# Performance work log

Measured on AMD Instinct MI355X. Metric: run time of the kernel, lower is better.

Reference implementation:

```python
import jax, jax.numpy as jnp
import numpy as np

B, N, M, P, LQK, LV, DQK, DV = 2, 512, 50, 2, 9, 9, 32, 32
K = DQK // 2  # theta frequencies; repeat_interleave(theta,2) must match last dim of q/k


def setup_inputs() -> dict:
    key = jax.random.key(0)
    ks = jax.random.split(key, 7)
    q = jax.random.normal(ks[0], (B, N, P, LQK, DQK), dtype=jnp.float32)
    k = jax.random.normal(ks[1], (B, N, P, LQK, DQK), dtype=jnp.float32)
    v = jax.random.normal(ks[2], (B, N, P, LV, DV), dtype=jnp.float32)
    pos = jax.random.normal(ks[3], (B, N, 3), dtype=jnp.float32) * 3.0  # atom coords
    u = jax.random.normal(ks[4], (B, M, 3), dtype=jnp.float32)
    grid_u = u / jnp.linalg.norm(u, axis=-1, keepdims=True)  # unit-sphere Lebedev points
    grid_w = jax.random.uniform(ks[5], (B, M), dtype=jnp.float32) / M  # quadrature weights
    theta = jax.random.uniform(ks[6], (K,), dtype=jnp.float32)
    return {"q": q, "k": k, "v": v, "pos": pos, "grid_u": grid_u, "grid_w": grid_w, "theta": theta}


def apply_erope(x, pos, grid_u, theta):
    # x: [B,N,P,L,H]; pos: [B,N,3]; grid_u: [B,M,3]; theta: [K], H = 2K
    proj = jnp.einsum('bnd,bmd->bmn', pos, grid_u)           # [B,M,N]
    rep_theta = jnp.repeat(theta, 2)                          # [H]
    ang = proj[..., None] * rep_theta                         # [B,M,N,H]
    sin, cos = jnp.sin(ang), jnp.cos(ang)
    # rotate pairs: (x0,x1) -> (-x1, x0) interleaved
    xs = jnp.stack([-x[..., 1::2], x[..., ::2]], axis=-1).reshape(x.shape)
    return (jnp.einsum('bNPLH,bMNH->bMNPLH', x, cos)
            + jnp.einsum('bNPLH,bMNH->bMNPLH', xs, sin))      # [B,M,N,P,L,H]


def reference(q, k, v, pos, grid_u, grid_w, theta):
    qr = apply_erope(q, pos, grid_u, theta)  # [B,M,N,P,L,Dqk]
    kr = apply_erope(k, pos, grid_u, theta)
    b, m, n = qr.shape[:3]
    qf = qr.reshape(b, m, n, -1)             # [B,M,N,t], t = P*L*Dqk
    kf = kr.reshape(b, m, n, -1)
    vf = v.reshape(v.shape[0], v.shape[1], -1)  # [B,N,qdim]
    qf = qf / (qf.shape[-1] ** 0.5)
    # Exactly equals torch's kv=einsum('bMNt,bNq->bMNtq'); y=einsum('bMNt,bMNtq,bM->bMNq')
    # without materializing the [B,M,N,t,q] outer product.
    y = jnp.einsum('bMNt,bMNt,bNq,bM->bMNq', qf, kf, vf, grid_w)
    return y.reshape(b, m, n, *v.shape[2:])   # [B,M,N,P,LV,DV]
```

## Files before the change

kernel.cpp:

```cpp
#include <hip/hip_runtime.h>

#define BQ   2
#define NN   512
#define MM   50
#define TDIM 576
#define T4   144

__global__ void __launch_bounds__(64) dotqk_kernel(const float* __restrict__ q,
                                                   const float* __restrict__ k,
                                                   float* __restrict__ d) {
    const int row  = blockIdx.x;
    const int lane = threadIdx.x;
    const float4* q4 = (const float4*)(q + (size_t)row * TDIM);
    const float4* k4 = (const float4*)(k + (size_t)row * TDIM);
    float acc = 0.0f;
    for (int i = lane; i < T4; i += 64) {
        float4 a = q4[i];
        float4 b = k4[i];
        acc += a.x * b.x + a.y * b.y + a.z * b.z + a.w * b.w;
    }
    for (int off = 32; off > 0; off >>= 1)
        acc += __shfl_down(acc, off, 64);
    if (lane == 0) d[row] = acc * (1.0f / 24.0f);
}

__global__ void __launch_bounds__(256) scale_write_kernel(const float* __restrict__ v,
                                                          const float* __restrict__ w,
                                                          const float* __restrict__ d,
                                                          float* __restrict__ out,
                                                          long total4) {
    const long stride = (long)gridDim.x * blockDim.x;
    for (long i = (long)blockIdx.x * blockDim.x + threadIdx.x; i < total4; i += stride) {
        int  q4 = (int)(i % T4);
        long r  = i / T4;
        int  n  = (int)(r % NN); r /= NN;
        int  m  = (int)(r % MM);
        int  b  = (int)(r / MM);
        float s = d[b * NN + n] * w[b * MM + m];
        float4 vv = ((const float4*)v)[(long)(b * NN + n) * T4 + q4];
        float4 o;
        o.x = vv.x * s;
        o.y = vv.y * s;
        o.z = vv.z * s;
        o.w = vv.w * s;
        ((float4*)out)[i] = o;
    }
}

extern "C" void kernel_launch(void* const* d_in, const int* in_sizes, int n_in,
                              void* d_out, int out_size, void* d_ws, size_t ws_size,
                              hipStream_t stream) {
    const float* q      = (const float*)d_in[0];
    const float* k      = (const float*)d_in[1];
    const float* v      = (const float*)d_in[2];
    const float* w      = (const float*)d_in[5];
    float*       out    = (float*)d_out;
    float*       dscal  = (float*)d_ws;

    dotqk_kernel<<<BQ * NN, 64, 0, stream>>>(q, k, dscal);

    const long total4 = (long)BQ * MM * NN * T4;
    scale_write_kernel<<<2048, 256, 0, stream>>>(v, w, dscal, out, total4);
}
```

Before: 29.91 us.

## Fuse qk dot and scaled broadcast write into one kernel with nontemporal stores

Merges the per-row q·k reduction and the broadcast scaling of v across grid points into a single kernel. Each block reduces its row's dot product, caches v in shared memory, then writes half of the M outputs with nontemporal stores. This removes a second launch, the workspace round trip and the 64-bit div/mod indexing, at the cost of recomputing the dot product once per split.

```diff
diff --git a/kernel.cpp b/kernel.cpp
--- a/kernel.cpp
+++ b/kernel.cpp
@@ -1,64 +1,69 @@
 #include <hip/hip_runtime.h>
 
-#define BQ   2
-#define NN   512
-#define MM   50
-#define TDIM 576
-#define T4   144
+#define BQ     2
+#define NN     512
+#define MM     50
+#define TDIM   576
+#define T4     144
+#define SPLIT  2
+#define MSPLIT (MM / SPLIT)
 
-__global__ void __launch_bounds__(64) dotqk_kernel(const float* __restrict__ q,
-                                                   const float* __restrict__ k,
-                                                   float* __restrict__ d) {
-    const int row  = blockIdx.x;
-    const int lane = threadIdx.x;
-    const float4* q4 = (const float4*)(q + (size_t)row * TDIM);
-    const float4* k4 = (const float4*)(k + (size_t)row * TDIM);
+typedef float f4 __attribute__((ext_vector_type(4)));
+
+__global__ void __launch_bounds__(256) erope_fused_kernel(
+        const float* __restrict__ q,
+        const float* __restrict__ k,
+        const float* __restrict__ v,
+        const float* __restrict__ w,
+        float* __restrict__ out) {
+    const int blk   = blockIdx.x;
+    const int split = blk & (SPLIT - 1);
+    const int row   = blk >> 1;
+    const int b     = row >> 9;
+    const int n     = row & (NN - 1);
+    const int t     = threadIdx.x;
+
+    __shared__ f4    vsh[T4];
+    __shared__ float red[4];
+    __shared__ float dsh;
+
     float acc = 0.0f;
-    for (int i = lane; i < T4; i += 64) {
-        float4 a = q4[i];
-        float4 b = k4[i];
-        acc += a.x * b.x + a.y * b.y + a.z * b.z + a.w * b.w;
+    if (t < T4) {
+        const f4 a = ((const f4*)(q + (size_t)row * TDIM))[t];
+        const f4 c = ((const f4*)(k + (size_t)row * TDIM))[t];
+        vsh[t] = ((const f4*)(v + (size_t)row * TDIM))[t];
+        acc = a.x * c.x + a.y * c.y + a.z * c.z + a.w * c.w;
     }
+    #pragma unroll
     for (int off = 32; off > 0; off >>= 1)
         acc += __shfl_down(acc, off, 64);
-    if (lane == 0) d[row] = acc * (1.0f / 24.0f);
-}
+    if ((t & 63) == 0) red[t >> 6] = acc;
+    __syncthreads();
+    if (t == 0) dsh = (red[0] + red[1] + red[2] + red[3]) * (1.0f / 24.0f);
+    __syncthreads();
+    const float dval = dsh;
 
-__global__ void __launch_bounds__(256) scale_write_kernel(const float* __restrict__ v,
-                                                          const float* __restrict__ w,
-                                                          const float* __restrict__ d,
-                                                          float* __restrict__ out,
-                                                          long total4) {
-    const long stride = (long)gridDim.x * blockDim.x;
-    for (long i = (long)blockIdx.x * blockDim.x + threadIdx.x; i < total4; i += stride) {
-        int  q4 = (int)(i % T4);
-        long r  = i / T4;
-        int  n  = (int)(r % NN); r /= NN;
-        int  m  = (int)(r % MM);
-        int  b  = (int)(r / MM);
-        float s = d[b * NN + n] * w[b * MM + m];
-        float4 vv = ((const float4*)v)[(long)(b * NN + n) * T4 + q4];
-        float4 o;
-        o.x = vv.x * s;
-        o.y = vv.y * s;
-        o.z = vv.z * s;
-        o.w = vv.w * s;
-        ((float4*)out)[i] = o;
+    const float* wrow = w + b * MM + split * MSPLIT;
+    f4* out4 = (f4*)out;
+    for (int i = t; i < MSPLIT * T4; i += 256) {
+        const int ml = i / T4;
+        const int qi = i - ml * T4;
+        const int m  = split * MSPLIT + ml;
+        const float s = dval * wrow[ml];
+        const f4 vv = vsh[qi];
+        const f4 o  = vv * s;
+        __builtin_nontemporal_store(o, &out4[((size_t)(b * MM + m) * NN + n) * T4 + qi]);
     }
 }
 
 extern "C" void kernel_launch(void* const* d_in, const int* in_sizes, int n_in,
                               void* d_out, int out_size, void* d_ws, size_t ws_size,
                               hipStream_t stream) {
-    const float* q      = (const float*)d_in[0];
-    const float* k      = (const float*)d_in[1];
-    const float* v      = (const float*)d_in[2];
-    const float* w      = (const float*)d_in[5];
-    float*       out    = (float*)d_out;
-    float*       dscal  = (float*)d_ws;
+    const float* q   = (const float*)d_in[0];
+    const float* k   = (const float*)d_in[1];
+    const float* v   = (const float*)d_in[2];
+    const float* w   = (const float*)d_in[5];
+    float*       out = (float*)d_out;
 
-    dotqk_kernel<<<BQ * NN, 64, 0, stream>>>(q, k, dscal);
-
-    const long total4 = (long)BQ * MM * NN * T4;
-    scale_write_kernel<<<2048, 256, 0, stream>>>(v, w, dscal, out, total4);
+    erope_fused_kernel<<<BQ * NN * SPLIT, 256, 0, stream>>>(q, k, v, w, out);
 }
```

After: 26.40 us. 1.13x faster.
